# Kernel tuning notes

Hardware: AMD Instinct MI355X
Metric: run time of the kernel (lower is better)

The kernel has to match this reference:

```python
import jax, jax.numpy as jnp
from jax import lax
import numpy as np

NUM_HEADS = 8
K_RATIO = 0.5
GN_EPS = 1e-6
CLAMP = 32.0          # fp32 branch of the torch code
FILL = -1e9           # fp32 masked-fill value
L2_EPS = 1e-12        # torch F.normalize eps


def setup_inputs() -> dict:
    key = jax.random.key(0)
    k1, k2, k3 = jax.random.split(key, 3)
    B, C, H, W = 1, 256, 64, 64
    x = jax.random.normal(k1, (B, C, H, W), dtype=jnp.float32)
    w_qkv = jax.random.normal(k2, (3 * C, C), dtype=jnp.float32) * 0.02  # 1x1 conv, no bias
    w_proj = jax.random.normal(k3, (C, C), dtype=jnp.float32) * 0.02     # 1x1 conv, no bias
    gamma = jnp.ones((C,), dtype=jnp.float32)   # GroupNorm affine
    beta = jnp.zeros((C,), dtype=jnp.float32)
    return {"x": x, "w_qkv": w_qkv, "w_proj": w_proj, "gamma": gamma, "beta": beta}


def _l2norm(t):
    n = jnp.sqrt(jnp.sum(t * t, axis=-1, keepdims=True))
    return t / jnp.maximum(n, L2_EPS)


def reference(x, w_qkv, w_proj, gamma, beta):
    B, C, H, W = x.shape
    N = H * W
    hd = C // NUM_HEADS
    scale = hd ** -0.5

    # qkv 1x1 conv -> [B, 3C, H, W] -> [B, 3, heads, hd, N]
    qkv = jnp.einsum('bchw,oc->bohw', x, w_qkv).reshape(B, 3, NUM_HEADS, hd, N)
    q = jnp.swapaxes(qkv[:, 0], -1, -2)  # [B, heads, N, hd]
    k = jnp.swapaxes(qkv[:, 1], -1, -2)
    v = jnp.swapaxes(qkv[:, 2], -1, -2)

    q = _l2norm(q)
    k = _l2norm(k)

    attn = jnp.einsum('bhnd,bhmd->bhnm', q, k) * scale  # [B, heads, N, N]
    attn = jnp.clip(attn, -CLAMP, CLAMP)

    k_num = max(int(N * K_RATIO), 1)
    if k_num < N:
        # keep only top-k per row; threshold at the k-th largest value
        # (equivalent to torch.topk + scatter mask for continuous-valued scores)
        kth = lax.top_k(attn, k_num)[0][..., -1:]
        attn = jnp.where(attn >= kth, attn, FILL)

    attn = jax.nn.softmax(attn, axis=-1)
    out = jnp.einsum('bhnm,bhmd->bhnd', attn, v)          # [B, heads, N, hd]
    out = jnp.swapaxes(out, -1, -2).reshape(B, C, H, W)   # transpose(2,3) + reshape

    out = jnp.einsum('bchw,oc->bohw', out, w_proj)        # proj 1x1 conv

    # GroupNorm(groups=min(32, C//4)=32, eps=1e-6) with affine
    G = min(32, C // 4)
    xg = out.reshape(B, G, -1)
    mean = jnp.mean(xg, axis=-1, keepdims=True)
    var = jnp.var(xg, axis=-1, keepdims=True)
    xg = (xg - mean) / jnp.sqrt(var + GN_EPS)
    out = xg.reshape(B, C, H, W) * gamma[None, :, None, None] + beta[None, :, None, None]
    return out
```

## Files before the change

### kernel.cpp

```cpp
#include <hip/hip_runtime.h>


#define NTOK 4096
#define HD 32
#define NHEADS 8
#define KSEL 2048
#define SCALE 0.17677669529663689f
#define LOG2C 7.73937f

typedef __fp16 f16x2 __attribute__((ext_vector_type(2)));

#define USE_DOT2 (__has_builtin(__builtin_amdgcn_fdot2) && \
                  __has_builtin(__builtin_amdgcn_cvt_pkrtz))


__device__ __forceinline__ unsigned fkey(float f) {
  unsigned b = __float_as_uint(f);
  return (b & 0x80000000u) ? ~b : (b | 0x80000000u);
}
__device__ __forceinline__ float unfkey(unsigned k) {
  unsigned b = (k & 0x80000000u) ? (k ^ 0x80000000u) : ~k;
  return __uint_as_float(b);
}
__device__ __forceinline__ unsigned rfl_u(unsigned x) {
  return __builtin_amdgcn_readfirstlane(x);
}
__device__ __forceinline__ f16x2 asv2h(unsigned u) {
  union { unsigned u; f16x2 h; } c; c.u = u; return c.h;
}
__device__ __forceinline__ unsigned asu32(f16x2 h) {
  union { f16x2 h; unsigned u; } c; c.h = h; return c.u;
}
__device__ __forceinline__ unsigned probe_rf(unsigned klo, unsigned khi,
                                             float xlo, float xhi,
                                             int clo, int chi) {
  float t = xlo + (xhi - xlo) * ((float)(clo - KSEL) / (float)(clo - chi));
  unsigned k = fkey(t);
  if (k <= klo) k = klo + 1u;
  if (k > khi) k = khi;
  return k;
}


template <bool SCATTER>
__global__ __launch_bounds__(256) void gemm_k256(
    const float* __restrict__ A, const float* __restrict__ B,
    float* __restrict__ C0, float* __restrict__ C1, float* __restrict__ C2) {
  __shared__ float Wt[64][17];
  __shared__ float Xt[16][64];

  const int tid = threadIdx.x;
  const int tx = tid & 15, ty = tid >> 4;
  const int o0 = blockIdx.y * 64, n0 = blockIdx.x * 64;

  const int wr = tid >> 2, wc = (tid & 3) << 2;
  const int xr = tid >> 4, xc = (tid & 15) << 2;

  float4 acc[4];
#pragma unroll
  for (int i = 0; i < 4; ++i) acc[i] = make_float4(0.f, 0.f, 0.f, 0.f);

  for (int k0 = 0; k0 < 256; k0 += 16) {
    float4 wv = *(const float4*)(A + (o0 + wr) * 256 + k0 + wc);
    float4 xv = *(const float4*)(B + (k0 + xr) * 4096 + n0 + xc);
    Wt[wr][wc + 0] = wv.x; Wt[wr][wc + 1] = wv.y;
    Wt[wr][wc + 2] = wv.z; Wt[wr][wc + 3] = wv.w;
    *(float4*)&Xt[xr][xc] = xv;
    __syncthreads();
#pragma unroll
    for (int kk = 0; kk < 16; ++kk) {
      float4 b = *(const float4*)&Xt[kk][tx << 2];
#pragma unroll
      for (int i = 0; i < 4; ++i) {
        float a = Wt[(ty << 2) + i][kk];
        acc[i].x += a * b.x; acc[i].y += a * b.y;
        acc[i].z += a * b.z; acc[i].w += a * b.w;
      }
    }
    __syncthreads();
  }

  if (SCATTER) {
#pragma unroll
    for (int i = 0; i < 4; ++i) {
      int o = o0 + (ty << 2) + i;
      int which = o >> 8, rem = o & 255;
      int h = rem >> 5, d = rem & 31;
      int n = n0 + (tx << 2);
      if (which == 1) {
        *(float4*)(C1 + h * (HD * NTOK) + d * NTOK + n) = acc[i];
      } else {
        float* dst = (which == 0) ? C0 : C2;
        int base = h * (NTOK * HD) + d;
        dst[base + (n + 0) * HD] = acc[i].x;
        dst[base + (n + 1) * HD] = acc[i].y;
        dst[base + (n + 2) * HD] = acc[i].z;
        dst[base + (n + 3) * HD] = acc[i].w;
      }
    }
  } else {
#pragma unroll
    for (int i = 0; i < 4; ++i) {
      int o = o0 + (ty << 2) + i;
      *(float4*)(C0 + o * 4096 + n0 + (tx << 2)) = acc[i];
    }
  }
}


__global__ __launch_bounds__(256) void l2norm_q(float* __restrict__ Q) {
  const int tid = threadIdx.x;
  const int p = blockIdx.x * 8 + (tid >> 5);
  const int d = tid & 31;
  const int idx = p * HD + d;
  float v = Q[idx];
  float ss = v * v;
#pragma unroll
  for (int m = 16; m >= 1; m >>= 1) ss += __shfl_xor(ss, m, 32);
  float nrm = sqrtf(ss);
  Q[idx] = v * SCALE / fmaxf(nrm, 1e-12f);
}


__global__ __launch_bounds__(256) void l2norm_kt_pack(float* __restrict__ KT) {
  const int n = blockIdx.x * 256 + threadIdx.x;
  float* P = KT + blockIdx.y * (HD * NTOK) + n;
  float v[HD];
  float ss = 0.f;
#pragma unroll
  for (int d = 0; d < HD; ++d) {
    v[d] = P[d * NTOK];
    ss += v[d] * v[d];
  }
  float inv = 1.f / fmaxf(sqrtf(ss), 1e-12f);
  unsigned* O = (unsigned*)P;
#pragma unroll
  for (int d2 = 0; d2 < 16; ++d2) {
#if USE_DOT2
    O[d2 * NTOK] = asu32(
        __builtin_amdgcn_cvt_pkrtz(v[2 * d2] * inv, v[2 * d2 + 1] * inv));
#else
    f16x2 p; p[0] = (__fp16)(v[2 * d2] * inv); p[1] = (__fp16)(v[2 * d2 + 1] * inv);
    O[d2 * NTOK] = asu32(p);
#endif
  }
}


__global__ __launch_bounds__(256, 5) void attn_kernel(
    const float* __restrict__ Q, const float* __restrict__ KT,
    const float* __restrict__ V, float* __restrict__ AO) {
  __shared__ __align__(16) unsigned char wtsT[NTOK][4];
  __shared__ float qs[128];
  __shared__ unsigned qs2u[4][16];
  __shared__ float pvred[4 * 8 * 4 * 4];
  __shared__ unsigned ired[2][4][2];
  __shared__ unsigned dred[4][4];

  const int tid = threadIdx.x;
  const int wv = tid >> 6, lane = tid & 63;
  const int head = blockIdx.x & 7;
  const int n0 = (blockIdx.x >> 3) << 2;

  const float* Qh = Q + head * (NTOK * HD);
  const float* KTh = KT + head * (HD * NTOK);
  const float* Vh = V + head * (NTOK * HD);

  if (tid < 128) qs[tid] = Qh[n0 * HD + tid];
  __syncthreads();
  if (tid < 64) {
    const int r = tid >> 4, d2 = tid & 15;
#if USE_DOT2
    qs2u[r][d2] = asu32(__builtin_amdgcn_cvt_pkrtz(
        qs[r * HD + (d2 << 1)], qs[r * HD + (d2 << 1) + 1]));
#else
    f16x2 p; p[0] = (__fp16)qs[r * HD + (d2 << 1)];
    p[1] = (__fp16)qs[r * HD + (d2 << 1) + 1];
    qs2u[r][d2] = asu32(p);
#endif
  }
  __syncthreads();

  float kr[4][16];
#pragma unroll
  for (int r = 0; r < 4; ++r)
#pragma unroll
    for (int j = 0; j < 16; ++j) kr[r][j] = 0.f;

  const int cb = tid << 2;
  const unsigned* k16 = (const unsigned*)KTh + cb;
#pragma unroll 1
  for (int d2 = 0; d2 < 16; ++d2) {
    const unsigned* kp = k16 + d2 * NTOK;
    const uint4 kv0 = *(const uint4*)(kp);
    const uint4 kv1 = *(const uint4*)(kp + 1024);
    const uint4 kv2 = *(const uint4*)(kp + 2048);
    const uint4 kv3 = *(const uint4*)(kp + 3072);
    const unsigned qu0 = qs2u[0][d2], qu1 = qs2u[1][d2];
    const unsigned qu2 = qs2u[2][d2], qu3 = qs2u[3][d2];
#if USE_DOT2
    const f16x2 q0 = asv2h(qu0), q1 = asv2h(qu1);
    const f16x2 q2 = asv2h(qu2), q3 = asv2h(qu3);
#define DOT16(r, qv)                                                         \
    kr[r][0]  = __builtin_amdgcn_fdot2(qv, asv2h(kv0.x), kr[r][0],  false);  \
    kr[r][1]  = __builtin_amdgcn_fdot2(qv, asv2h(kv0.y), kr[r][1],  false);  \
    kr[r][2]  = __builtin_amdgcn_fdot2(qv, asv2h(kv0.z), kr[r][2],  false);  \
    kr[r][3]  = __builtin_amdgcn_fdot2(qv, asv2h(kv0.w), kr[r][3],  false);  \
    kr[r][4]  = __builtin_amdgcn_fdot2(qv, asv2h(kv1.x), kr[r][4],  false);  \
    kr[r][5]  = __builtin_amdgcn_fdot2(qv, asv2h(kv1.y), kr[r][5],  false);  \
    kr[r][6]  = __builtin_amdgcn_fdot2(qv, asv2h(kv1.z), kr[r][6],  false);  \
    kr[r][7]  = __builtin_amdgcn_fdot2(qv, asv2h(kv1.w), kr[r][7],  false);  \
    kr[r][8]  = __builtin_amdgcn_fdot2(qv, asv2h(kv2.x), kr[r][8],  false);  \
    kr[r][9]  = __builtin_amdgcn_fdot2(qv, asv2h(kv2.y), kr[r][9],  false);  \
    kr[r][10] = __builtin_amdgcn_fdot2(qv, asv2h(kv2.z), kr[r][10], false);  \
    kr[r][11] = __builtin_amdgcn_fdot2(qv, asv2h(kv2.w), kr[r][11], false);  \
    kr[r][12] = __builtin_amdgcn_fdot2(qv, asv2h(kv3.x), kr[r][12], false);  \
    kr[r][13] = __builtin_amdgcn_fdot2(qv, asv2h(kv3.y), kr[r][13], false);  \
    kr[r][14] = __builtin_amdgcn_fdot2(qv, asv2h(kv3.z), kr[r][14], false);  \
    kr[r][15] = __builtin_amdgcn_fdot2(qv, asv2h(kv3.w), kr[r][15], false);
    DOT16(0, q0) DOT16(1, q1) DOT16(2, q2) DOT16(3, q3)
#undef DOT16
#else
#define DOTF(r, qu)                                                          \
    {                                                                        \
      const f16x2 qq = asv2h(qu);                                            \
      const float qa = (float)qq[0], qb = (float)qq[1];                      \
      const unsigned kk[16] = {kv0.x, kv0.y, kv0.z, kv0.w, kv1.x, kv1.y,     \
                               kv1.z, kv1.w, kv2.x, kv2.y, kv2.z, kv2.w,     \
                               kv3.x, kv3.y, kv3.z, kv3.w};                  \
      _Pragma("unroll")                                                      \
      for (int j = 0; j < 16; ++j) {                                         \
        const f16x2 kh = asv2h(kk[j]);                                       \
        kr[r][j] += qa * (float)kh[0] + qb * (float)kh[1];                   \
      }                                                                      \
    }
    DOTF(0, qu0) DOTF(1, qu1) DOTF(2, qu2) DOTF(3, qu3)
#undef DOTF
#endif
  }

  unsigned klo0 = 0x417FFFFFu, khi0 = 0xBE800000u;
  unsigned klo1 = 0x417FFFFFu, khi1 = 0xBE800000u;
  unsigned klo2 = 0x417FFFFFu, khi2 = 0xBE800000u;
  unsigned klo3 = 0x417FFFFFu, khi3 = 0xBE800000u;
  float xlo0 = -0.25f, xhi0 = 0.25f, xlo1 = -0.25f, xhi1 = 0.25f;
  float xlo2 = -0.25f, xhi2 = 0.25f, xlo3 = -0.25f, xhi3 = 0.25f;
  int clo0 = NTOK, chi0 = 0, clo1 = NTOK, chi1 = 0;
  int clo2 = NTOK, chi2 = 0, clo3 = NTOK, chi3 = 0;
  bool dn0 = false, dn1 = false, dn2 = false, dn3 = false;
  int slot = 0;
#pragma unroll 1
  for (int it = 0; it < 40; ++it) {
    unsigned m0 = dn0 ? klo0
        : ((it < 8 && (khi0 - klo0) > 65536u)
               ? rfl_u(probe_rf(klo0, khi0, xlo0, xhi0, clo0, chi0))
               : klo0 + ((khi0 - klo0 + 1u) >> 1));
    unsigned m1 = dn1 ? klo1
        : ((it < 8 && (khi1 - klo1) > 65536u)
               ? rfl_u(probe_rf(klo1, khi1, xlo1, xhi1, clo1, chi1))
               : klo1 + ((khi1 - klo1 + 1u) >> 1));
    unsigned m2 = dn2 ? klo2
        : ((it < 8 && (khi2 - klo2) > 65536u)
               ? rfl_u(probe_rf(klo2, khi2, xlo2, xhi2, clo2, chi2))
               : klo2 + ((khi2 - klo2 + 1u) >> 1));
    unsigned m3 = dn3 ? klo3
        : ((it < 8 && (khi3 - klo3) > 65536u)
               ? rfl_u(probe_rf(klo3, khi3, xlo3, xhi3, clo3, chi3))
               : klo3 + ((khi3 - klo3 + 1u) >> 1));
    unsigned c0 = 0, c1 = 0, c2 = 0, c3 = 0;
    if (!dn0) {
      const float f0 = unfkey(m0);
#pragma unroll
      for (int j = 0; j < 16; ++j) c0 += __popcll(__ballot(kr[0][j] >= f0));
    }
    if (!dn1) {
      const float f1 = unfkey(m1);
#pragma unroll
      for (int j = 0; j < 16; ++j) c1 += __popcll(__ballot(kr[1][j] >= f1));
    }
    if (!dn2) {
      const float f2 = unfkey(m2);
#pragma unroll
      for (int j = 0; j < 16; ++j) c2 += __popcll(__ballot(kr[2][j] >= f2));
    }
    if (!dn3) {
      const float f3 = unfkey(m3);
#pragma unroll
      for (int j = 0; j < 16; ++j) c3 += __popcll(__ballot(kr[3][j] >= f3));
    }
    if (lane == 0) {
      ired[slot][wv][0] = c0 | (c1 << 16);
      ired[slot][wv][1] = c2 | (c3 << 16);
    }
    __syncthreads();
    unsigned a01 = rfl_u(ired[slot][0][0] + ired[slot][1][0] +
                         ired[slot][2][0] + ired[slot][3][0]);
    unsigned a23 = rfl_u(ired[slot][0][1] + ired[slot][1][1] +
                         ired[slot][2][1] + ired[slot][3][1]);
    slot ^= 1;
    int C0 = (int)(a01 & 0xFFFFu), C1 = (int)(a01 >> 16);
    int C2 = (int)(a23 & 0xFFFFu), C3 = (int)(a23 >> 16);
#define BUPD(C, klo, khi, xlo, xhi, clo, chi, dn, mk)                        \
    if (!dn) {                                                               \
      if (C == KSEL) { klo = mk; dn = true; }                                \
      else if (C > KSEL) { klo = mk; xlo = unfkey(mk); clo = C; }            \
      else { khi = mk - 1u; xhi = unfkey(mk); chi = C; }                     \
      if (klo >= khi) dn = true;                                             \
    }
    BUPD(C0, klo0, khi0, xlo0, xhi0, clo0, chi0, dn0, m0)
    BUPD(C1, klo1, khi1, xlo1, xhi1, clo1, chi1, dn1, m1)
    BUPD(C2, klo2, khi2, xlo2, xhi2, clo2, chi2, dn2, m2)
    BUPD(C3, klo3, khi3, xlo3, xhi3, clo3, chi3, dn3, m3)
#undef BUPD
    if (dn0 && dn1 && dn2 && dn3) break;
  }
  const float tf0 = unfkey(klo0), tf1 = unfkey(klo1);
  const float tf2 = unfkey(klo2), tf3 = unfkey(klo3);

  unsigned id0 = 0, id1 = 0, id2 = 0, id3 = 0;
#pragma unroll
  for (int g = 0; g < 4; ++g) {
    unsigned pk[4];
#pragma unroll
    for (int t = 0; t < 4; ++t) {
      const int j = (g << 2) + t;
      float s0 = kr[0][j], s1 = kr[1][j], s2 = kr[2][j], s3 = kr[3][j];
      unsigned u0 = (s0 >= tf0) ? (unsigned)rintf(exp2f(__builtin_fmaf(s0, 1.44269504f, LOG2C))) : 0u;
      unsigned u1 = (s1 >= tf1) ? (unsigned)rintf(exp2f(__builtin_fmaf(s1, 1.44269504f, LOG2C))) : 0u;
      unsigned u2 = (s2 >= tf2) ? (unsigned)rintf(exp2f(__builtin_fmaf(s2, 1.44269504f, LOG2C))) : 0u;
      unsigned u3 = (s3 >= tf3) ? (unsigned)rintf(exp2f(__builtin_fmaf(s3, 1.44269504f, LOG2C))) : 0u;
      id0 += u0; id1 += u1; id2 += u2; id3 += u3;
      pk[t] = u0 | (u1 << 8) | (u2 << 16) | (u3 << 24);
    }
    const int col = (g << 10) + cb;
    *(uint4*)&wtsT[col][0] = make_uint4(pk[0], pk[1], pk[2], pk[3]);
  }
#pragma unroll
  for (int s = 1; s < 64; s <<= 1) {
    id0 += __shfl_xor(id0, s); id1 += __shfl_xor(id1, s);
    id2 += __shfl_xor(id2, s); id3 += __shfl_xor(id3, s);
  }
  if (lane == 0) *(uint4*)&dred[wv][0] = make_uint4(id0, id1, id2, id3);
  __syncthreads();
  const float dnm0 = (float)(dred[0][0] + dred[1][0] + dred[2][0] + dred[3][0]);
  const float dnm1 = (float)(dred[0][1] + dred[1][1] + dred[2][1] + dred[3][1]);
  const float dnm2 = (float)(dred[0][2] + dred[1][2] + dred[2][2] + dred[3][2]);
  const float dnm3 = (float)(dred[0][3] + dred[1][3] + dred[2][3] + dred[3][3]);

  const int slot5 = lane & 7, mg = lane >> 3;
  const int mbase = wv << 10;
  float av[4][4];
#pragma unroll
  for (int r = 0; r < 4; ++r)
#pragma unroll
    for (int c = 0; c < 4; ++c) av[r][c] = 0.f;

#pragma unroll 4
  for (int ii = 0; ii < 128; ++ii) {
    const int m = mbase + (ii << 3) + mg;
    unsigned wq = *(const unsigned*)&wtsT[m][0];
    float4 v = *(const float4*)(Vh + m * HD + (slot5 << 2));
    float w0 = (float)(wq & 0xFFu);
    float w1 = (float)((wq >> 8) & 0xFFu);
    float w2 = (float)((wq >> 16) & 0xFFu);
    float w3 = (float)(wq >> 24);
    av[0][0] += w0 * v.x; av[0][1] += w0 * v.y; av[0][2] += w0 * v.z; av[0][3] += w0 * v.w;
    av[1][0] += w1 * v.x; av[1][1] += w1 * v.y; av[1][2] += w1 * v.z; av[1][3] += w1 * v.w;
    av[2][0] += w2 * v.x; av[2][1] += w2 * v.y; av[2][2] += w2 * v.z; av[2][3] += w2 * v.w;
    av[3][0] += w3 * v.x; av[3][1] += w3 * v.y; av[3][2] += w3 * v.z; av[3][3] += w3 * v.w;
  }
#pragma unroll
  for (int r = 0; r < 4; ++r)
#pragma unroll
    for (int c = 0; c < 4; ++c) {
      float x = av[r][c];
      x += __shfl_xor(x, 8); x += __shfl_xor(x, 16); x += __shfl_xor(x, 32);
      av[r][c] = x;
    }
  if (mg == 0) {
#pragma unroll
    for (int r = 0; r < 4; ++r)
#pragma unroll
      for (int c = 0; c < 4; ++c)
        pvred[(((wv << 3) + slot5) * 4 + r) * 4 + c] = av[r][c];
  }
  __syncthreads();

  if (tid < 128) {
    const int r = tid >> 5, d = tid & 31;
    const int sl = d >> 2, c = d & 3;
    float val = 0.f;
#pragma unroll
    for (int w = 0; w < 4; ++w) val += pvred[(((w << 3) + sl) * 4 + r) * 4 + c];
    float dn = (r == 0) ? dnm0 : (r == 1) ? dnm1 : (r == 2) ? dnm2 : dnm3;
    val /= dn;
    AO[(head * HD + d) * NTOK + n0 + r] = val;
  }
}


__global__ __launch_bounds__(256) void gn_stats(const float* __restrict__ O,
                                                float* __restrict__ ST) {
  const int g = blockIdx.x, tid = threadIdx.x;
  const float4* p4 = (const float4*)(O + g * 32768);
  float s = 0.f, ss = 0.f;
  for (int i = tid; i < 8192; i += 256) {
    float4 v = p4[i];
    s += (v.x + v.y) + (v.z + v.w);
    ss += (v.x * v.x + v.y * v.y) + (v.z * v.z + v.w * v.w);
  }
#pragma unroll
  for (int m = 1; m < 64; m <<= 1) {
    s += __shfl_xor(s, m);
    ss += __shfl_xor(ss, m);
  }
  __shared__ float rs[4], rss[4];
  if ((tid & 63) == 0) { rs[tid >> 6] = s; rss[tid >> 6] = ss; }
  __syncthreads();
  if (tid == 0) {
    float S = rs[0] + rs[1] + rs[2] + rs[3];
    float SS = rss[0] + rss[1] + rss[2] + rss[3];
    float mean = S * (1.f / 32768.f);
    float var = SS * (1.f / 32768.f) - mean * mean;
    ST[g * 2] = mean;
    ST[g * 2 + 1] = rsqrtf(var + 1e-6f);
  }
}


__global__ __launch_bounds__(256) void gn_apply(float* __restrict__ O,
                                                const float* __restrict__ ST,
                                                const float* __restrict__ gamma,
                                                const float* __restrict__ beta) {
  const int i4 = blockIdx.x * 256 + threadIdx.x;
  const int c = i4 >> 10, g = c >> 3;
  const float a = ST[g * 2 + 1] * gamma[c];
  const float b = beta[c] - ST[g * 2] * a;
  float4 v = *(float4*)(O + (i4 << 2));
  v.x = v.x * a + b; v.y = v.y * a + b; v.z = v.z * a + b; v.w = v.w * a + b;
  *(float4*)(O + (i4 << 2)) = v;
}


extern "C" void kernel_launch(void* const* d_in, const int* in_sizes, int n_in,
                              void* d_out, int out_size, void* d_ws,
                              size_t ws_size, hipStream_t stream) {
  const float* x = (const float*)d_in[0];
  const float* w_qkv = (const float*)d_in[1];
  const float* w_proj = (const float*)d_in[2];
  const float* gamma = (const float*)d_in[3];
  const float* beta = (const float*)d_in[4];
  float* out = (float*)d_out;

  float* Q = (float*)d_ws;
  float* KT = Q + 1048576;
  float* V = KT + 1048576;
  float* AO = V + 1048576;
  float* ST = AO + 1048576;

  gemm_k256<true><<<dim3(64, 12), 256, 0, stream>>>(w_qkv, x, Q, KT, V);
  l2norm_q<<<4096, 256, 0, stream>>>(Q);
  l2norm_kt_pack<<<dim3(16, 8), 256, 0, stream>>>(KT);
  attn_kernel<<<8192, 256, 0, stream>>>(Q, KT, V, AO);
  gemm_k256<false><<<dim3(64, 4), 256, 0, stream>>>(w_proj, AO, out, nullptr, nullptr);
  gn_stats<<<32, 256, 0, stream>>>(out, ST);
  gn_apply<<<1024, 256, 0, stream>>>(out, ST, gamma, beta);
}
```

Baseline: 452.8 us.

## Store V in fp16 and accumulate attention-weighted V with packed half math

The QKV GEMM now writes V as fp16. The attention kernel stores its quantized softmax weights as fp16 in LDS and runs the weight-times-V loop with packed f16x2 multiply-adds, converting to fp32 only before the cross-lane reduction. This halves the V bytes read per block and doubles arithmetic per instruction in the PV loop. In exchange, accumulation over 128 steps in fp16 loses precision and could approach overflow for large partial sums.

Measured after the change: 444.3 us. About the same (-1.9%).

```diff
diff --git a/kernel.cpp b/kernel.cpp
--- a/kernel.cpp
+++ b/kernel.cpp
@@ -30,6 +30,20 @@
 }
 __device__ __forceinline__ unsigned asu32(f16x2 h) {
   union { f16x2 h; unsigned u; } c; c.h = h; return c.u;
+}
+__device__ __forceinline__ unsigned dup_lo16(unsigned x) {
+#if __has_builtin(__builtin_amdgcn_perm)
+  return __builtin_amdgcn_perm(x, x, 0x05040504u);
+#else
+  return (x & 0xFFFFu) | (x << 16);
+#endif
+}
+__device__ __forceinline__ unsigned dup_hi16(unsigned x) {
+#if __has_builtin(__builtin_amdgcn_perm)
+  return __builtin_amdgcn_perm(x, x, 0x07060706u);
+#else
+  return (x & 0xFFFF0000u) | (x >> 16);
+#endif
 }
 __device__ __forceinline__ unsigned probe_rf(unsigned klo, unsigned khi,
                                              float xlo, float xhi,
@@ -89,13 +103,19 @@
       int n = n0 + (tx << 2);
       if (which == 1) {
         *(float4*)(C1 + h * (HD * NTOK) + d * NTOK + n) = acc[i];
+      } else if (which == 2) {
+        __fp16* vh = (__fp16*)C2;
+        int base = h * (NTOK * HD) + d;
+        vh[base + (n + 0) * HD] = (__fp16)acc[i].x;
+        vh[base + (n + 1) * HD] = (__fp16)acc[i].y;
+        vh[base + (n + 2) * HD] = (__fp16)acc[i].z;
+        vh[base + (n + 3) * HD] = (__fp16)acc[i].w;
       } else {
-        float* dst = (which == 0) ? C0 : C2;
         int base = h * (NTOK * HD) + d;
-        dst[base + (n + 0) * HD] = acc[i].x;
-        dst[base + (n + 1) * HD] = acc[i].y;
-        dst[base + (n + 2) * HD] = acc[i].z;
-        dst[base + (n + 3) * HD] = acc[i].w;
+        C0[base + (n + 0) * HD] = acc[i].x;
+        C0[base + (n + 1) * HD] = acc[i].y;
+        C0[base + (n + 2) * HD] = acc[i].z;
+        C0[base + (n + 3) * HD] = acc[i].w;
       }
     }
   } else {
@@ -149,8 +169,8 @@
 
 __global__ __launch_bounds__(256, 5) void attn_kernel(
     const float* __restrict__ Q, const float* __restrict__ KT,
-    const float* __restrict__ V, float* __restrict__ AO) {
-  __shared__ __align__(16) unsigned char wtsT[NTOK][4];
+    const __fp16* __restrict__ V16, float* __restrict__ AO) {
+  __shared__ __align__(16) __fp16 wts2[NTOK][4];
   __shared__ float qs[128];
   __shared__ unsigned qs2u[4][16];
   __shared__ float pvred[4 * 8 * 4 * 4];
@@ -164,7 +184,7 @@
 
   const float* Qh = Q + head * (NTOK * HD);
   const float* KTh = KT + head * (HD * NTOK);
-  const float* Vh = V + head * (NTOK * HD);
+  const __fp16* Vh = V16 + head * (NTOK * HD);
 
   if (tid < 128) qs[tid] = Qh[n0 * HD + tid];
   __syncthreads();
@@ -320,20 +340,28 @@
   unsigned id0 = 0, id1 = 0, id2 = 0, id3 = 0;
 #pragma unroll
   for (int g = 0; g < 4; ++g) {
-    unsigned pk[4];
+    unsigned pk[8];
 #pragma unroll
     for (int t = 0; t < 4; ++t) {
       const int j = (g << 2) + t;
       float s0 = kr[0][j], s1 = kr[1][j], s2 = kr[2][j], s3 = kr[3][j];
-      unsigned u0 = (s0 >= tf0) ? (unsigned)rintf(exp2f(__builtin_fmaf(s0, 1.44269504f, LOG2C))) : 0u;
-      unsigned u1 = (s1 >= tf1) ? (unsigned)rintf(exp2f(__builtin_fmaf(s1, 1.44269504f, LOG2C))) : 0u;
-      unsigned u2 = (s2 >= tf2) ? (unsigned)rintf(exp2f(__builtin_fmaf(s2, 1.44269504f, LOG2C))) : 0u;
-      unsigned u3 = (s3 >= tf3) ? (unsigned)rintf(exp2f(__builtin_fmaf(s3, 1.44269504f, LOG2C))) : 0u;
-      id0 += u0; id1 += u1; id2 += u2; id3 += u3;
-      pk[t] = u0 | (u1 << 8) | (u2 << 16) | (u3 << 24);
+      float u0 = (s0 >= tf0) ? rintf(exp2f(__builtin_fmaf(s0, 1.44269504f, LOG2C))) : 0.f;
+      float u1 = (s1 >= tf1) ? rintf(exp2f(__builtin_fmaf(s1, 1.44269504f, LOG2C))) : 0.f;
+      float u2 = (s2 >= tf2) ? rintf(exp2f(__builtin_fmaf(s2, 1.44269504f, LOG2C))) : 0.f;
+      float u3 = (s3 >= tf3) ? rintf(exp2f(__builtin_fmaf(s3, 1.44269504f, LOG2C))) : 0.f;
+      id0 += (unsigned)u0; id1 += (unsigned)u1;
+      id2 += (unsigned)u2; id3 += (unsigned)u3;
+#if USE_DOT2
+      pk[(t << 1) + 0] = asu32(__builtin_amdgcn_cvt_pkrtz(u0, u1));
+      pk[(t << 1) + 1] = asu32(__builtin_amdgcn_cvt_pkrtz(u2, u3));
+#else
+      { f16x2 a; a[0] = (__fp16)u0; a[1] = (__fp16)u1; pk[(t << 1) + 0] = asu32(a); }
+      { f16x2 b; b[0] = (__fp16)u2; b[1] = (__fp16)u3; pk[(t << 1) + 1] = asu32(b); }
+#endif
     }
     const int col = (g << 10) + cb;
-    *(uint4*)&wtsT[col][0] = make_uint4(pk[0], pk[1], pk[2], pk[3]);
+    *(uint4*)&wts2[col][0]     = make_uint4(pk[0], pk[1], pk[2], pk[3]);
+    *(uint4*)&wts2[col + 2][0] = make_uint4(pk[4], pk[5], pk[6], pk[7]);
   }
 #pragma unroll
   for (int s = 1; s < 64; s <<= 1) {
@@ -349,25 +377,32 @@
 
   const int slot5 = lane & 7, mg = lane >> 3;
   const int mbase = wv << 10;
-  float av[4][4];
+  f16x2 av2[4][2];
 #pragma unroll
   for (int r = 0; r < 4; ++r)
 #pragma unroll
-    for (int c = 0; c < 4; ++c) av[r][c] = 0.f;
+    for (int c = 0; c < 2; ++c) { av2[r][c][0] = (__fp16)0.f; av2[r][c][1] = (__fp16)0.f; }
 
 #pragma unroll 4
   for (int ii = 0; ii < 128; ++ii) {
     const int m = mbase + (ii << 3) + mg;
-    unsigned wq = *(const unsigned*)&wtsT[m][0];
-    float4 v = *(const float4*)(Vh + m * HD + (slot5 << 2));
-    float w0 = (float)(wq & 0xFFu);
-    float w1 = (float)((wq >> 8) & 0xFFu);
-    float w2 = (float)((wq >> 16) & 0xFFu);
-    float w3 = (float)(wq >> 24);
-    av[0][0] += w0 * v.x; av[0][1] += w0 * v.y; av[0][2] += w0 * v.z; av[0][3] += w0 * v.w;
-    av[1][0] += w1 * v.x; av[1][1] += w1 * v.y; av[1][2] += w1 * v.z; av[1][3] += w1 * v.w;
-    av[2][0] += w2 * v.x; av[2][1] += w2 * v.y; av[2][2] += w2 * v.z; av[2][3] += w2 * v.w;
-    av[3][0] += w3 * v.x; av[3][1] += w3 * v.y; av[3][2] += w3 * v.z; av[3][3] += w3 * v.w;
+    const uint2 wq = *(const uint2*)&wts2[m][0];
+    const uint2 vv = *(const uint2*)(Vh + m * HD + (slot5 << 2));
+    const f16x2 va = asv2h(vv.x), vb = asv2h(vv.y);
+    const f16x2 w00 = asv2h(dup_lo16(wq.x));
+    const f16x2 w11 = asv2h(dup_hi16(wq.x));
+    const f16x2 w22 = asv2h(dup_lo16(wq.y));
+    const f16x2 w33 = asv2h(dup_hi16(wq.y));
+    av2[0][0] += w00 * va; av2[0][1] += w00 * vb;
+    av2[1][0] += w11 * va; av2[1][1] += w11 * vb;
+    av2[2][0] += w22 * va; av2[2][1] += w22 * vb;
+    av2[3][0] += w33 * va; av2[3][1] += w33 * vb;
+  }
+  float av[4][4];
+#pragma unroll
+  for (int r = 0; r < 4; ++r) {
+    av[r][0] = (float)av2[r][0][0]; av[r][1] = (float)av2[r][0][1];
+    av[r][2] = (float)av2[r][1][0]; av[r][3] = (float)av2[r][1][1];
   }
 #pragma unroll
   for (int r = 0; r < 4; ++r)
@@ -454,14 +489,14 @@
 
   float* Q = (float*)d_ws;
   float* KT = Q + 1048576;
-  float* V = KT + 1048576;
-  float* AO = V + 1048576;
+  float* V16r = KT + 1048576;
+  float* AO = V16r + 1048576;
   float* ST = AO + 1048576;
 
-  gemm_k256<true><<<dim3(64, 12), 256, 0, stream>>>(w_qkv, x, Q, KT, V);
+  gemm_k256<true><<<dim3(64, 12), 256, 0, stream>>>(w_qkv, x, Q, KT, V16r);
   l2norm_q<<<4096, 256, 0, stream>>>(Q);
   l2norm_kt_pack<<<dim3(16, 8), 256, 0, stream>>>(KT);
-  attn_kernel<<<8192, 256, 0, stream>>>(Q, KT, V, AO);
+  attn_kernel<<<8192, 256, 0, stream>>>(Q, KT, (const __fp16*)V16r, AO);
   gemm_k256<false><<<dim3(64, 4), 256, 0, stream>>>(w_proj, AO, out, nullptr, nullptr);
   gn_stats<<<32, 256, 0, stream>>>(out, ST);
   gn_apply<<<1024, 256, 0, stream>>>(out, ST, gamma, beta);
```
